# Kernel tuning notes

Measured on AMD Instinct MI355X. Metric: run time of the kernel, lower is better.

The kernel has to match this reference:

```python
import jax, jax.numpy as jnp
import numpy as np
from jax import lax

B, CIN, H, W = 8, 64, 128, 128
COUT, K = 128, 3
PAD, STRIDE, DIL = 1, 1, 1
KK = K * K


def setup_inputs() -> dict:
    ks = jax.random.split(jax.random.key(0), 6)
    x = jax.random.normal(ks[0], (B, CIN, H, W), jnp.float32)
    pre_w = jax.random.normal(ks[1], (CIN, CIN, 1, 1), jnp.float32) * (1.0 / float(np.sqrt(CIN)))
    pre_b = jnp.zeros((CIN,), jnp.float32)
    off_w = jax.random.normal(ks[2], (2 * KK, CIN, K, K), jnp.float32) * 0.01
    off_b = jnp.zeros((2 * KK,), jnp.float32)
    mod_w = jax.random.normal(ks[3], (KK, CIN, K, K), jnp.float32) * 0.01
    mod_b = jnp.zeros((KK,), jnp.float32)
    reg_w = jax.random.normal(ks[4], (COUT, CIN, K, K), jnp.float32) * (1.0 / float(np.sqrt(CIN * KK)))
    return dict(x=x, pre_w=pre_w, pre_b=pre_b, off_w=off_w, off_b=off_b,
                mod_w=mod_w, mod_b=mod_b, reg_w=reg_w)


def _conv3x3(x, w, b):
    y = lax.conv_general_dilated(x, w, (STRIDE, STRIDE), [(PAD, PAD), (PAD, PAD)],
                                 rhs_dilation=(DIL, DIL),
                                 dimension_numbers=('NCHW', 'OIHW', 'NCHW'))
    return y + b[None, :, None, None]


def _bilinear(img, py, px):
    # img: [C,H,W]; py,px: [KK,Ho,Wo] float coords; zero padding outside image
    Hh, Ww = img.shape[1], img.shape[2]
    y0f = jnp.floor(py)
    x0f = jnp.floor(px)
    wy = py - y0f
    wx = px - x0f
    y0 = y0f.astype(jnp.int32)
    x0 = x0f.astype(jnp.int32)

    def gather(yi, xi):
        valid = (yi >= 0) & (yi < Hh) & (xi >= 0) & (xi < Ww)
        yc = jnp.clip(yi, 0, Hh - 1)
        xc = jnp.clip(xi, 0, Ww - 1)
        return img[:, yc, xc] * valid[None].astype(img.dtype)  # [C,KK,Ho,Wo]

    return (gather(y0, x0) * ((1 - wy) * (1 - wx))[None]
            + gather(y0, x0 + 1) * ((1 - wy) * wx)[None]
            + gather(y0 + 1, x0) * (wy * (1 - wx))[None]
            + gather(y0 + 1, x0 + 1) * (wy * wx)[None])


def _dcn_forward(x, pre_w, pre_b, off_w, off_b, mod_w, mod_b, reg_w):
    # 1x1 channel-mapping conv created in the original forward
    x = lax.conv_general_dilated(x, pre_w, (1, 1), 'VALID',
                                 dimension_numbers=('NCHW', 'OIHW', 'NCHW'))
    x = x + pre_b[None, :, None, None]

    offset = _conv3x3(x, off_w, off_b)                    # [B,2*KK,Ho,Wo]
    mask = 2.0 * jax.nn.sigmoid(_conv3x3(x, mod_w, mod_b))  # [B,KK,Ho,Wo]

    Ho, Wo = offset.shape[2], offset.shape[3]
    off = offset.reshape(B, KK, 2, Ho, Wo)  # torchvision layout: per kernel pos (dy,dx)

    ky, kx = jnp.meshgrid(jnp.arange(K), jnp.arange(K), indexing='ij')
    base_y = (jnp.arange(Ho) * STRIDE - PAD)[None, :, None] + (ky.reshape(KK) * DIL)[:, None, None]  # [KK,Ho,1]
    base_x = (jnp.arange(Wo) * STRIDE - PAD)[None, None, :] + (kx.reshape(KK) * DIL)[:, None, None]  # [KK,1,Wo]

    py = base_y[None].astype(x.dtype) + off[:, :, 0]  # [B,KK,Ho,Wo]
    px = base_x[None].astype(x.dtype) + off[:, :, 1]

    sampled = jax.vmap(_bilinear)(x, py, px)          # [B,C,KK,Ho,Wo]
    sampled = sampled * mask[:, None]                  # modulation

    wk = reg_w.reshape(COUT, CIN, KK)
    return jnp.einsum('bckhw,ock->bohw', sampled, wk)  # [B,COUT,Ho,Wo]


def reference(x, pre_w, pre_b, off_w, off_b, mod_w, mod_b, reg_w):
    return _dcn_forward(x, pre_w, pre_b, off_w, off_b, mod_w, mod_b, reg_w)
```

## Files before the change

kernel.cpp:

```cpp
#include <hip/hip_runtime.h>
#include <hip/hip_bf16.h>
#include <cstdint>
#include <cstddef>

#define BATCH 8
#define CINC  64
#define HH    128
#define WWW   128
#define COUTC 128
#define KKC   9
#define KDIM  576
#define HWC   (HH*WWW)
#define NPX   (BATCH*HWC)

#define AT_BASE 98304
#define AT_SZ   32768

typedef float f32x4 __attribute__((ext_vector_type(4)));
typedef short bf16x8 __attribute__((ext_vector_type(8)));

static __device__ __forceinline__ unsigned short f2bf(float f){
    unsigned u = __builtin_bit_cast(unsigned, f);
    u += 0x7fffu + ((u >> 16) & 1u);
    return (unsigned short)(u >> 16);
}
static __device__ __forceinline__ float bf_lo(unsigned u){
    return __builtin_bit_cast(float, u << 16);
}
static __device__ __forceinline__ float bf_hi(unsigned u){
    return __builtin_bit_cast(float, u & 0xffff0000u);
}
static __device__ __forceinline__ unsigned cvtpk(float lo, float hi){
    unsigned r;
    asm("v_cvt_pk_bf16_f32 %0, %1, %2" : "=v"(r) : "v"(lo), "v"(hi));
    return r;
}

__global__ __launch_bounds__(256) void prep_weights(
        const float* __restrict__ off_w, const float* __restrict__ mod_w,
        const float* __restrict__ reg_w, const float* __restrict__ pre_w,
        unsigned short* __restrict__ Wb, unsigned short* __restrict__ Wc,
        unsigned short* __restrict__ Wp)
{
    int idx = blockIdx.x * 256 + threadIdx.x;
    if (idx < COUTC * KDIM) {
        int o = idx / KDIM, k = idx % KDIM;
        int kk = k >> 6, c = k & 63;
        Wb[idx] = f2bf(reg_w[(o * CINC + c) * KKC + kk]);
    }
    int idx2 = idx - COUTC * KDIM;
    if (idx2 >= 0 && idx2 < 32 * KDIM) {
        int o = idx2 / KDIM, k = idx2 % KDIM;
        int kk = k >> 6, c = k & 63;
        float v = 0.f;
        if (o < 18)      v = off_w[(o * CINC + c) * KKC + kk];
        else if (o < 27) v = mod_w[((o - 18) * CINC + c) * KKC + kk];
        Wc[idx2] = f2bf(v);
    }
    int idx3 = idx - (COUTC * KDIM + 32 * KDIM);
    if (idx3 >= 0 && idx3 < CINC * CINC)
        Wp[idx3] = f2bf(pre_w[idx3]);
}

__global__ __launch_bounds__(256) void conv1x1(
        const float* __restrict__ x, const unsigned short* __restrict__ Wp,
        const float* __restrict__ pre_b, unsigned short* __restrict__ xp)
{
    __shared__ unsigned short slab[4][64 * 72];

    const int tid = threadIdx.x;
    const int lane = tid & 63;
    const int wv   = tid >> 6;
    const int l15  = lane & 15;
    const int l4   = lane >> 4;

    int bid = (int)blockIdx.x;
    int bswz = (bid & 7) * 64 + (bid >> 3);
    int pxb = bswz * 256 + wv * 64;
    int b = pxb >> 14, hw0 = pxb & 16383;
    const float* xb = x + (size_t)b * CINC * HWC + hw0;

    bf16x8 bw[4][2];
    #pragma unroll
    for (int fn = 0; fn < 4; ++fn)
        #pragma unroll
        for (int s = 0; s < 2; ++s)
            bw[fn][s] = *(const bf16x8*)(Wp + (size_t)(16*fn + l15) * 64 + 32*s + 8*l4);
    float pb[4];
    #pragma unroll
    for (int fn = 0; fn < 4; ++fn) pb[fn] = pre_b[16*fn + l15];

    f32x4 acc[4][4];
    #pragma unroll
    for (int su = 0; su < 4; ++su)
        #pragma unroll
        for (int fn = 0; fn < 4; ++fn) acc[su][fn] = (f32x4){0.f,0.f,0.f,0.f};

    #pragma unroll
    for (int su = 0; su < 4; ++su) {
        #pragma unroll
        for (int s = 0; s < 2; ++s) {
            float f[8];
            #pragma unroll
            for (int j = 0; j < 8; ++j)
                f[j] = xb[(size_t)(s*32 + 8*l4 + j) * HWC + su*16 + l15];
            unsigned pk[4];
            #pragma unroll
            for (int d = 0; d < 4; ++d) pk[d] = cvtpk(f[2*d], f[2*d+1]);
            bf16x8 A = __builtin_bit_cast(bf16x8, make_uint4(pk[0], pk[1], pk[2], pk[3]));
            #pragma unroll
            for (int fn = 0; fn < 4; ++fn)
                acc[su][fn] = __builtin_amdgcn_mfma_f32_16x16x32_bf16(A, bw[fn][s], acc[su][fn], 0,0,0);
        }
    }

    unsigned short* sl = slab[wv];
    #pragma unroll
    for (int su = 0; su < 4; ++su)
        #pragma unroll
        for (int fn = 0; fn < 4; ++fn)
            #pragma unroll
            for (int r = 0; r < 4; ++r)
                sl[(su*16 + 4*l4 + r) * 72 + 16*fn + l15] = f2bf(acc[su][fn][r] + pb[fn]);
    const uint4* srow = (const uint4*)(sl + lane * 72);
    uint4* drow = (uint4*)(xp + (size_t)(pxb + lane) * 64);
    #pragma unroll
    for (int q = 0; q < 8; ++q) drow[q] = srow[q];
}

__global__ __launch_bounds__(512, 2) void gather_einsum(
        const unsigned short* __restrict__ xp,
        const unsigned short* __restrict__ Wb,
        const unsigned short* __restrict__ Wc,
        const float* __restrict__ off_b,
        const float* __restrict__ mod_b,
        float* __restrict__ out)
{
    __shared__ char smem[163840];
    char* winc = smem;
    float* epi = (float*)smem;

    const int tid  = (int)threadIdx.x;
    const int lane = tid & 63;
    const int wv   = tid >> 6;
    const int l15  = lane & 15;
    const int l4   = lane >> 4;

    int bid = (int)blockIdx.x;
    int bswz = (bid & 7) * 64 + (bid >> 3);
    const int b  = bswz >> 6;
    const int h0 = (bswz & 63) * 2;

    const unsigned short* xpb = xp + (size_t)b * HWC * CINC;

    #pragma unroll
    for (int i = 0; i < 12; ++i) {
        int c = i * 512 + tid;
        int r = c >> 10;
        int c10 = c & 1023;
        int xph = c10 >> 3, g = c10 & 7;
        int y = h0 - 2 + r;
        uint4 v = make_uint4(0u,0u,0u,0u);
        if ((unsigned)y < 128u)
            v = *(const uint4*)(xpb + ((size_t)y * 128 + xph) * 64 + g * 8);
        *(uint4*)(winc + (r*128 + xph)*128 + ((g ^ (xph & 7)) << 4)) = v;
    }
    __syncthreads();

    const int hrow = wv >> 2;
    const int x0w  = (wv & 3) * 32;
    {
        f32x4 aco[2][2];
        #pragma unroll
        for (int j = 0; j < 2; ++j)
            #pragma unroll
            for (int fn = 0; fn < 2; ++fn) aco[j][fn] = (f32x4){0.f,0.f,0.f,0.f};

        #pragma unroll
        for (int kk = 0; kk < 9; ++kk) {
            bf16x8 bc0[2], bc1[2];
            #pragma unroll
            for (int fn = 0; fn < 2; ++fn) {
                bc0[fn] = *(const bf16x8*)(Wc + (size_t)(16*fn + l15) * KDIM + kk*64 + 8*l4);
                bc1[fn] = *(const bf16x8*)(Wc + (size_t)(16*fn + l15) * KDIM + kk*64 + 32 + 8*l4);
            }
            int wr_ = hrow + (kk / 3) + 1;
            #pragma unroll
            for (int j = 0; j < 2; ++j) {
                int xx = x0w + j*16 + l15 + (kk % 3) - 1;
                bool xv = (unsigned)xx < 128u;
                int xc = xx < 0 ? 0 : (xx > 127 ? 127 : xx);
                int sx = xc & 7;
                const char* rr = winc + (wr_*128 + xc)*128;
                uint4 a0 = *(const uint4*)(rr + ((l4 ^ sx) << 4));
                uint4 a1 = *(const uint4*)(rr + (((l4+4) ^ sx) << 4));
                if (!xv) { a0 = make_uint4(0,0,0,0); a1 = make_uint4(0,0,0,0); }
                bf16x8 A0 = __builtin_bit_cast(bf16x8, a0);
                bf16x8 A1 = __builtin_bit_cast(bf16x8, a1);
                #pragma unroll
                for (int fn = 0; fn < 2; ++fn) {
                    aco[j][fn] = __builtin_amdgcn_mfma_f32_16x16x32_bf16(A0, bc0[fn], aco[j][fn], 0,0,0);
                    aco[j][fn] = __builtin_amdgcn_mfma_f32_16x16x32_bf16(A1, bc1[fn], aco[j][fn], 0,0,0);
                }
            }
        }
        float* Dt = (float*)(smem + AT_BASE);
        #pragma unroll
        for (int j = 0; j < 2; ++j)
        #pragma unroll
        for (int fn = 0; fn < 2; ++fn) {
            int o = 16*fn + l15;
            #pragma unroll
            for (int r = 0; r < 4; ++r) {
                int pr = 4*l4 + r;
                int px = wv*32 + j*16 + pr;
                float v = aco[j][fn][r];
                if (o < 18) {
                    v += off_b[o];
                    int k = o >> 1;
                    if ((o & 1) == 0) v += (float)(h0 + hrow - 1 + k/3);
                    else              v += (float)(x0w + j*16 + pr - 1 + (k % 3));
                } else if (o < 27) {
                    v = 2.f / (1.f + __expf(-(v + mod_b[o - 18])));
                }
                if (o < 27) Dt[px*29 + o] = v;
            }
        }
    }
    __syncthreads();

    float cy[2][9], cx[2][9], cm[2][9];
    {
        const float* Dt = (const float*)(smem + AT_BASE);
        #pragma unroll
        for (int j = 0; j < 2; ++j) {
            int px = wv*32 + j*16 + l15;
            #pragma unroll
            for (int kk = 0; kk < 9; ++kk) {
                cy[j][kk] = Dt[px*29 + 2*kk];
                cx[j][kk] = Dt[px*29 + 2*kk + 1];
                cm[j][kk] = Dt[px*29 + 18 + kk];
            }
        }
    }
    __syncthreads();

    f32x4 acc[8][2];
    #pragma unroll
    for (int m = 0; m < 8; ++m) { acc[m][0] = (f32x4){0.f,0.f,0.f,0.f};
                                  acc[m][1] = (f32x4){0.f,0.f,0.f,0.f}; }

    const int wr = wv >> 2, wc = wv & 3;
    const unsigned short* wrow = Wb + (size_t)(32*wc + l15) * KDIM + 8*l4;
    const int sw  = l15 & 7;
    const int ao1 = (l4 ^ sw) << 4, ao2 = ((l4 + 4) ^ sw) << 4;

    #define LERP_TILE(kk_)  do {                                              \
        char* Ab = smem + AT_BASE + ((kk_) & 1) * AT_SZ;                      \
        _Pragma("unroll")                                                     \
        for (int j = 0; j < 2; ++j) {                                         \
            float Y = cy[j][kk_], X = cx[j][kk_], M = cm[j][kk_];             \
            float yf = floorf(Y), xf = floorf(X);                             \
            float wy = Y - yf, wx = X - xf;                                   \
            int y0 = (int)yf, x0i = (int)xf;                                  \
            int y1 = y0 + 1, x1 = x0i + 1;                                    \
            bool yv0 = (unsigned)y0 < 128u, yv1 = (unsigned)y1 < 128u;        \
            bool xv0 = (unsigned)x0i < 128u, xv1 = (unsigned)x1 < 128u;       \
            int xc0 = x0i < 0 ? 0 : (x0i > 127 ? 127 : x0i);                  \
            int xc1 = x1  < 0 ? 0 : (x1  > 127 ? 127 : x1);                   \
            int wr0 = y0 - (h0 - 2), wr1 = wr0 + 1;                           \
            int wc0 = wr0 < 0 ? 0 : (wr0 > 5 ? 5 : wr0);                      \
            int wc1 = wr1 < 0 ? 0 : (wr1 > 5 ? 5 : wr1);                      \
            int s0 = xc0 & 7, s1 = xc1 & 7;                                   \
            const char* r00 = winc + (wc0*128 + xc0)*128;                     \
            const char* r01 = winc + (wc0*128 + xc1)*128;                     \
            const char* r10 = winc + (wc1*128 + xc0)*128;                     \
            const char* r11 = winc + (wc1*128 + xc1)*128;                     \
            uint4 cb0 = *(const uint4*)(r00 + ((l4 ^ s0) << 4));              \
            uint4 cb1 = *(const uint4*)(r00 + (((l4+4) ^ s0) << 4));          \
            uint4 cb2 = *(const uint4*)(r01 + ((l4 ^ s1) << 4));              \
            uint4 cb3 = *(const uint4*)(r01 + (((l4+4) ^ s1) << 4));          \
            uint4 cb4 = *(const uint4*)(r10 + ((l4 ^ s0) << 4));              \
            uint4 cb5 = *(const uint4*)(r10 + (((l4+4) ^ s0) << 4));          \
            uint4 cb6 = *(const uint4*)(r11 + ((l4 ^ s1) << 4));              \
            uint4 cb7 = *(const uint4*)(r11 + (((l4+4) ^ s1) << 4));          \
            bool oob = (yv0 && (unsigned)wr0 > 5u) || (yv1 && (unsigned)wr1 > 5u); \
            if (__builtin_expect(oob, 0)) {                                   \
                int yc0 = y0 < 0 ? 0 : (y0 > 127 ? 127 : y0);                 \
                int yc1 = y1 < 0 ? 0 : (y1 > 127 ? 127 : y1);                 \
                const unsigned short* p00 = xpb + (size_t)(yc0*128 + xc0)*64 + 8*l4; \
                const unsigned short* p01 = xpb + (size_t)(yc0*128 + xc1)*64 + 8*l4; \
                const unsigned short* p10 = xpb + (size_t)(yc1*128 + xc0)*64 + 8*l4; \
                const unsigned short* p11 = xpb + (size_t)(yc1*128 + xc1)*64 + 8*l4; \
                cb0 = *(const uint4*)(p00);  cb1 = *(const uint4*)(p00 + 32); \
                cb2 = *(const uint4*)(p01);  cb3 = *(const uint4*)(p01 + 32); \
                cb4 = *(const uint4*)(p10);  cb5 = *(const uint4*)(p10 + 32); \
                cb6 = *(const uint4*)(p11);  cb7 = *(const uint4*)(p11 + 32); \
            }                                                                 \
            float u00 = (1.f - wy) * (1.f - wx) * M * ((yv0 && xv0) ? 1.f : 0.f); \
            float u01 = (1.f - wy) * wx         * M * ((yv0 && xv1) ? 1.f : 0.f); \
            float u10 = wy * (1.f - wx)         * M * ((yv1 && xv0) ? 1.f : 0.f); \
            float u11 = wy * wx                 * M * ((yv1 && xv1) ? 1.f : 0.f); \
            unsigned pk0[4], pk1[4];                                          \
            _Pragma("unroll")                                                 \
            for (int d = 0; d < 4; ++d) {                                     \
                unsigned q00, q01, q10, q11;                                  \
                q00 = cb0[d]; q01 = cb2[d]; q10 = cb4[d]; q11 = cb6[d];       \
                {                                                             \
                    float slo = bf_lo(q00)*u00 + bf_lo(q01)*u01 + bf_lo(q10)*u10 + bf_lo(q11)*u11; \
                    float shi = bf_hi(q00)*u00 + bf_hi(q01)*u01 + bf_hi(q10)*u10 + bf_hi(q11)*u11; \
                    pk0[d] = cvtpk(slo, shi);                                 \
                }                                                             \
                q00 = cb1[d]; q01 = cb3[d]; q10 = cb5[d]; q11 = cb7[d];       \
                {                                                             \
                    float slo = bf_lo(q00)*u00 + bf_lo(q01)*u01 + bf_lo(q10)*u10 + bf_lo(q11)*u11; \
                    float shi = bf_hi(q00)*u00 + bf_hi(q01)*u01 + bf_hi(q10)*u10 + bf_hi(q11)*u11; \
                    pk1[d] = cvtpk(slo, shi);                                 \
                }                                                             \
            }                                                                 \
            int pxl = wv*32 + j*16 + l15;                                     \
            char* ab = Ab + pxl*128;                                          \
            *(uint4*)(ab + ao1) = make_uint4(pk0[0], pk0[1], pk0[2], pk0[3]); \
            *(uint4*)(ab + ao2) = make_uint4(pk1[0], pk1[1], pk1[2], pk1[3]); \
        }                                                                     \
    } while (0)

    #define GEMM_STEP(g_)  do {                                               \
        const char* Ab = smem + AT_BASE + ((g_) & 1) * AT_SZ;                 \
        bf16x8 Bf00 = *(const bf16x8*)(wrow + (g_)*64);                       \
        bf16x8 Bf01 = *(const bf16x8*)(wrow + (g_)*64 + 32);                  \
        bf16x8 Bf10 = *(const bf16x8*)(wrow + (size_t)16*KDIM + (g_)*64);     \
        bf16x8 Bf11 = *(const bf16x8*)(wrow + (size_t)16*KDIM + (g_)*64 + 32);\
        _Pragma("unroll")                                                     \
        for (int m = 0; m < 8; ++m) {                                         \
            const char* ar = Ab + (128*wr + 16*m + l15)*128;                  \
            bf16x8 A0 = *(const bf16x8*)(ar + ao1);                           \
            bf16x8 A1 = *(const bf16x8*)(ar + ao2);                           \
            acc[m][0] = __builtin_amdgcn_mfma_f32_16x16x32_bf16(A0, Bf00, acc[m][0], 0,0,0); \
            acc[m][0] = __builtin_amdgcn_mfma_f32_16x16x32_bf16(A1, Bf01, acc[m][0], 0,0,0); \
            acc[m][1] = __builtin_amdgcn_mfma_f32_16x16x32_bf16(A0, Bf10, acc[m][1], 0,0,0); \
            acc[m][1] = __builtin_amdgcn_mfma_f32_16x16x32_bf16(A1, Bf11, acc[m][1], 0,0,0); \
        }                                                                     \
    } while (0)

    LERP_TILE(0);
    __syncthreads();
    #pragma unroll 1
    for (int kk = 1; kk < 9; ++kk) {
        LERP_TILE(kk);
        GEMM_STEP(kk - 1);
        __syncthreads();
    }
    GEMM_STEP(8);
    __syncthreads();

    #undef LERP_TILE
    #undef GEMM_STEP

    #pragma unroll
    for (int m = 0; m < 8; ++m)
        #pragma unroll
        for (int f = 0; f < 2; ++f)
            *(f32x4*)(epi + (size_t)(32*wc + 16*f + l15) * 260 + 128*wr + 16*m + 4*l4) = acc[m][f];
    __syncthreads();

    float* ob = out + (size_t)b * COUTC * HWC + h0 * 128;
    #pragma unroll
    for (int it = 0; it < 16; ++it) {
        int idx = it * 512 + tid;
        int o = idx >> 6, c = idx & 63;
        f32x4 v = *(const f32x4*)(epi + (size_t)o * 260 + 4*c);
        *(f32x4*)(ob + (size_t)o * HWC + 4*c) = v;
    }
}

extern "C" void kernel_launch(void* const* d_in, const int* in_sizes, int n_in,
                              void* d_out, int out_size, void* d_ws, size_t ws_size,
                              hipStream_t stream)
{
    const float* x     = (const float*)d_in[0];
    const float* pre_w = (const float*)d_in[1];
    const float* pre_b = (const float*)d_in[2];
    const float* off_w = (const float*)d_in[3];
    const float* off_b = (const float*)d_in[4];
    const float* mod_w = (const float*)d_in[5];
    const float* mod_b = (const float*)d_in[6];
    const float* reg_w = (const float*)d_in[7];
    float* out = (float*)d_out;

    unsigned short* xp = (unsigned short*)d_ws;
    unsigned short* Wb = (unsigned short*)((char*)d_ws + 16777216);
    unsigned short* Wc = (unsigned short*)((char*)d_ws + 16924672);
    unsigned short* Wp = (unsigned short*)((char*)d_ws + 16961536);

    prep_weights<<<dim3(376), dim3(256), 0, stream>>>(off_w, mod_w, reg_w, pre_w, Wb, Wc, Wp);
    conv1x1     <<<dim3(512), dim3(256), 0, stream>>>(x, Wp, pre_b, xp);
    gather_einsum<<<dim3(512), dim3(512), 0, stream>>>(xp, Wb, Wc, off_b, mod_b, out);
}
```

Measured before the change: 103.9 us.

## Halve gather_einsum tile width to fit two blocks per CU

The fused deformable-conv kernel now tiles 2 rows x 64 columns per block with 256 threads and 1024 blocks, instead of 2 rows x 128 columns with 512 threads. The LDS input window and the epilogue buffer shrink so that two independent blocks can share a CU, letting one block's barriers and sampling overlap with another's MFMA work. The offset/mask 3x3 conv now reads its inputs straight from global memory rather than the LDS window. In exchange, the 64-wide window has no horizontal halo, so samples at tile column edges fall into the slower global-memory gather path, and the offset-conv loads lose LDS reuse.

```diff
diff --git a/kernel.cpp b/kernel.cpp
--- a/kernel.cpp
+++ b/kernel.cpp
@@ -13,8 +13,11 @@
 #define HWC   (HH*WWW)
 #define NPX   (BATCH*HWC)
 
-#define AT_BASE 98304
-#define AT_SZ   32768
+#define WIN_W   64
+#define WIN_SZ  (6*WIN_W*128)
+#define AT_BASE WIN_SZ
+#define AT_SZ   (128*128)
+#define LDS_SZ  (WIN_SZ + 2*AT_SZ)
 
 typedef float f32x4 __attribute__((ext_vector_type(4)));
 typedef short bf16x8 __attribute__((ext_vector_type(8)));
@@ -128,7 +131,7 @@
     for (int q = 0; q < 8; ++q) drow[q] = srow[q];
 }
 
-__global__ __launch_bounds__(512, 2) void gather_einsum(
+__global__ __launch_bounds__(256, 2) void gather_einsum(
         const unsigned short* __restrict__ xp,
         const unsigned short* __restrict__ Wb,
         const unsigned short* __restrict__ Wc,
@@ -136,7 +139,7 @@
         const float* __restrict__ mod_b,
         float* __restrict__ out)
 {
-    __shared__ char smem[163840];
+    __shared__ char smem[LDS_SZ];
     char* winc = smem;
     float* epi = (float*)smem;
 
@@ -147,28 +150,29 @@
     const int l4   = lane >> 4;
 
     int bid = (int)blockIdx.x;
-    int bswz = (bid & 7) * 64 + (bid >> 3);
-    const int b  = bswz >> 6;
-    const int h0 = (bswz & 63) * 2;
+    int bswz = (bid & 7) * 128 + (bid >> 3);
+    const int b   = bswz >> 7;
+    const int rem = bswz & 127;
+    const int h0  = (rem >> 1) << 1;
+    const int x0w = (rem & 1) << 6;
 
     const unsigned short* xpb = xp + (size_t)b * HWC * CINC;
 
     #pragma unroll
     for (int i = 0; i < 12; ++i) {
-        int c = i * 512 + tid;
-        int r = c >> 10;
-        int c10 = c & 1023;
-        int xph = c10 >> 3, g = c10 & 7;
+        int c = i * 256 + tid;
+        int r = c >> 9;
+        int cr = c & 511;
+        int wx = cr >> 3, g = cr & 7;
         int y = h0 - 2 + r;
         uint4 v = make_uint4(0u,0u,0u,0u);
         if ((unsigned)y < 128u)
-            v = *(const uint4*)(xpb + ((size_t)y * 128 + xph) * 64 + g * 8);
-        *(uint4*)(winc + (r*128 + xph)*128 + ((g ^ (xph & 7)) << 4)) = v;
-    }
-    __syncthreads();
-
-    const int hrow = wv >> 2;
-    const int x0w  = (wv & 3) * 32;
+            v = *(const uint4*)(xpb + ((size_t)y * 128 + x0w + wx) * 64 + g * 8);
+        *(uint4*)(winc + (r*WIN_W + wx)*128 + ((g ^ (wx & 7)) << 4)) = v;
+    }
+
+    const int hrow = wv >> 1;
+    const int xsl  = (wv & 1) * 32;
     {
         f32x4 aco[2][2];
         #pragma unroll
@@ -184,17 +188,17 @@
                 bc0[fn] = *(const bf16x8*)(Wc + (size_t)(16*fn + l15) * KDIM + kk*64 + 8*l4);
                 bc1[fn] = *(const bf16x8*)(Wc + (size_t)(16*fn + l15) * KDIM + kk*64 + 32 + 8*l4);
             }
-            int wr_ = hrow + (kk / 3) + 1;
+            int y = h0 + hrow + kk/3 - 1;
+            bool yv = (unsigned)y < 128u;
             #pragma unroll
             for (int j = 0; j < 2; ++j) {
-                int xx = x0w + j*16 + l15 + (kk % 3) - 1;
-                bool xv = (unsigned)xx < 128u;
-                int xc = xx < 0 ? 0 : (xx > 127 ? 127 : xx);
-                int sx = xc & 7;
-                const char* rr = winc + (wr_*128 + xc)*128;
-                uint4 a0 = *(const uint4*)(rr + ((l4 ^ sx) << 4));
-                uint4 a1 = *(const uint4*)(rr + (((l4+4) ^ sx) << 4));
-                if (!xv) { a0 = make_uint4(0,0,0,0); a1 = make_uint4(0,0,0,0); }
+                int gx = x0w + xsl + j*16 + l15 + kk%3 - 1;
+                bool val = yv && ((unsigned)gx < 128u);
+                const uint4* src = (const uint4*)(xpb
+                    + ((size_t)((y & 127) * 128 + (gx & 127))) * 64 + 8 * l4);
+                uint4 z = make_uint4(0u,0u,0u,0u);
+                uint4 a0 = val ? src[0] : z;
+                uint4 a1 = val ? src[4] : z;
                 bf16x8 A0 = __builtin_bit_cast(bf16x8, a0);
                 bf16x8 A1 = __builtin_bit_cast(bf16x8, a1);
                 #pragma unroll
@@ -213,17 +217,17 @@
             #pragma unroll
             for (int r = 0; r < 4; ++r) {
                 int pr = 4*l4 + r;
-                int px = wv*32 + j*16 + pr;
+                int p  = hrow*64 + xsl + j*16 + pr;
                 float v = aco[j][fn][r];
                 if (o < 18) {
                     v += off_b[o];
                     int k = o >> 1;
                     if ((o & 1) == 0) v += (float)(h0 + hrow - 1 + k/3);
-                    else              v += (float)(x0w + j*16 + pr - 1 + (k % 3));
+                    else              v += (float)(x0w + xsl + j*16 + pr - 1 + (k % 3));
                 } else if (o < 27) {
                     v = 2.f / (1.f + __expf(-(v + mod_b[o - 18])));
                 }
-                if (o < 27) Dt[px*29 + o] = v;
+                if (o < 27) Dt[p*29 + o] = v;
             }
         }
     }
@@ -234,12 +238,12 @@
         const float* Dt = (const float*)(smem + AT_BASE);
         #pragma unroll
         for (int j = 0; j < 2; ++j) {
-            int px = wv*32 + j*16 + l15;
+            int p = wv*32 + j*16 + l15;
             #pragma unroll
             for (int kk = 0; kk < 9; ++kk) {
-                cy[j][kk] = Dt[px*29 + 2*kk];
-                cx[j][kk] = Dt[px*29 + 2*kk + 1];
-                cm[j][kk] = Dt[px*29 + 18 + kk];
+                cy[j][kk] = Dt[p*29 + 2*kk];
+                cx[j][kk] = Dt[p*29 + 2*kk + 1];
+                cm[j][kk] = Dt[p*29 + 18 + kk];
             }
         }
     }
@@ -250,8 +254,7 @@
     for (int m = 0; m < 8; ++m) { acc[m][0] = (f32x4){0.f,0.f,0.f,0.f};
                                   acc[m][1] = (f32x4){0.f,0.f,0.f,0.f}; }
 
-    const int wr = wv >> 2, wc = wv & 3;
-    const unsigned short* wrow = Wb + (size_t)(32*wc + l15) * KDIM + 8*l4;
+    const unsigned short* wrow = Wb + (size_t)(32*wv + l15) * KDIM + 8*l4;
     const int sw  = l15 & 7;
     const int ao1 = (l4 ^ sw) << 4, ao2 = ((l4 + 4) ^ sw) << 4;
 
@@ -266,16 +269,19 @@
             int y1 = y0 + 1, x1 = x0i + 1;                                    \
             bool yv0 = (unsigned)y0 < 128u, yv1 = (unsigned)y1 < 128u;        \
             bool xv0 = (unsigned)x0i < 128u, xv1 = (unsigned)x1 < 128u;       \
-            int xc0 = x0i < 0 ? 0 : (x0i > 127 ? 127 : x0i);                  \
-            int xc1 = x1  < 0 ? 0 : (x1  > 127 ? 127 : x1);                   \
             int wr0 = y0 - (h0 - 2), wr1 = wr0 + 1;                           \
+            int wxi = x0i - x0w;                                              \
+            bool inW0 = (unsigned)wxi < (unsigned)WIN_W;                      \
+            bool inW1 = (unsigned)(wxi + 1) < (unsigned)WIN_W;                \
             int wc0 = wr0 < 0 ? 0 : (wr0 > 5 ? 5 : wr0);                      \
             int wc1 = wr1 < 0 ? 0 : (wr1 > 5 ? 5 : wr1);                      \
-            int s0 = xc0 & 7, s1 = xc1 & 7;                                   \
-            const char* r00 = winc + (wc0*128 + xc0)*128;                     \
-            const char* r01 = winc + (wc0*128 + xc1)*128;                     \
-            const char* r10 = winc + (wc1*128 + xc0)*128;                     \
-            const char* r11 = winc + (wc1*128 + xc1)*128;                     \
+            int wx0 = wxi < 0 ? 0 : (wxi > WIN_W-1 ? WIN_W-1 : wxi);          \
+            int wx1 = wxi+1 < 0 ? 0 : (wxi+1 > WIN_W-1 ? WIN_W-1 : wxi+1);    \
+            int s0 = wx0 & 7, s1 = wx1 & 7;                                   \
+            const char* r00 = winc + (wc0*WIN_W + wx0)*128;                   \
+            const char* r01 = winc + (wc0*WIN_W + wx1)*128;                   \
+            const char* r10 = winc + (wc1*WIN_W + wx0)*128;                   \
+            const char* r11 = winc + (wc1*WIN_W + wx1)*128;                   \
             uint4 cb0 = *(const uint4*)(r00 + ((l4 ^ s0) << 4));              \
             uint4 cb1 = *(const uint4*)(r00 + (((l4+4) ^ s0) << 4));          \
             uint4 cb2 = *(const uint4*)(r01 + ((l4 ^ s1) << 4));              \
@@ -284,10 +290,13 @@
             uint4 cb5 = *(const uint4*)(r10 + (((l4+4) ^ s0) << 4));          \
             uint4 cb6 = *(const uint4*)(r11 + ((l4 ^ s1) << 4));              \
             uint4 cb7 = *(const uint4*)(r11 + (((l4+4) ^ s1) << 4));          \
-            bool oob = (yv0 && (unsigned)wr0 > 5u) || (yv1 && (unsigned)wr1 > 5u); \
+            bool oob = (yv0 && (unsigned)wr0 > 5u) || (yv1 && (unsigned)wr1 > 5u) \
+                    || (xv0 && !inW0) || (xv1 && !inW1);                      \
             if (__builtin_expect(oob, 0)) {                                   \
                 int yc0 = y0 < 0 ? 0 : (y0 > 127 ? 127 : y0);                 \
                 int yc1 = y1 < 0 ? 0 : (y1 > 127 ? 127 : y1);                 \
+                int xc0 = x0i < 0 ? 0 : (x0i > 127 ? 127 : x0i);              \
+                int xc1 = x1  < 0 ? 0 : (x1  > 127 ? 127 : x1);               \
                 const unsigned short* p00 = xpb + (size_t)(yc0*128 + xc0)*64 + 8*l4; \
                 const unsigned short* p01 = xpb + (size_t)(yc0*128 + xc1)*64 + 8*l4; \
                 const unsigned short* p10 = xpb + (size_t)(yc1*128 + xc0)*64 + 8*l4; \
@@ -318,8 +327,8 @@
                     pk1[d] = cvtpk(slo, shi);                                 \
                 }                                                             \
             }                                                                 \
-            int pxl = wv*32 + j*16 + l15;                                     \
-            char* ab = Ab + pxl*128;                                          \
+            int p = wv*32 + j*16 + l15;                                       \
+            char* ab = Ab + p*128;                                            \
             *(uint4*)(ab + ao1) = make_uint4(pk0[0], pk0[1], pk0[2], pk0[3]); \
             *(uint4*)(ab + ao2) = make_uint4(pk1[0], pk1[1], pk1[2], pk1[3]); \
         }                                                                     \
@@ -333,7 +342,7 @@
         bf16x8 Bf11 = *(const bf16x8*)(wrow + (size_t)16*KDIM + (g_)*64 + 32);\
         _Pragma("unroll")                                                     \
         for (int m = 0; m < 8; ++m) {                                         \
-            const char* ar = Ab + (128*wr + 16*m + l15)*128;                  \
+            const char* ar = Ab + (16*m + l15)*128;                           \
             bf16x8 A0 = *(const bf16x8*)(ar + ao1);                           \
             bf16x8 A1 = *(const bf16x8*)(ar + ao2);                           \
             acc[m][0] = __builtin_amdgcn_mfma_f32_16x16x32_bf16(A0, Bf00, acc[m][0], 0,0,0); \
@@ -361,16 +370,17 @@
     for (int m = 0; m < 8; ++m)
         #pragma unroll
         for (int f = 0; f < 2; ++f)
-            *(f32x4*)(epi + (size_t)(32*wc + 16*f + l15) * 260 + 128*wr + 16*m + 4*l4) = acc[m][f];
+            *(f32x4*)(epi + (size_t)(32*wv + 16*f + l15) * 130 + 16*m + 4*l4) = acc[m][f];
     __syncthreads();
 
-    float* ob = out + (size_t)b * COUTC * HWC + h0 * 128;
+    float* ob = out + (size_t)b * COUTC * HWC + h0 * 128 + x0w;
     #pragma unroll
     for (int it = 0; it < 16; ++it) {
-        int idx = it * 512 + tid;
-        int o = idx >> 6, c = idx & 63;
-        f32x4 v = *(const f32x4*)(epi + (size_t)o * 260 + 4*c);
-        *(f32x4*)(ob + (size_t)o * HWC + 4*c) = v;
+        int idx = it * 256 + tid;
+        int o = idx >> 5, q = idx & 31;
+        int p = 4 * q;
+        f32x4 v = *(const f32x4*)(epi + (size_t)o * 130 + p);
+        *(f32x4*)(ob + (size_t)o * HWC + (p >> 6) * 128 + (p & 63)) = v;
     }
 }
 
@@ -395,5 +405,5 @@
 
     prep_weights<<<dim3(376), dim3(256), 0, stream>>>(off_w, mod_w, reg_w, pre_w, Wb, Wc, Wp);
     conv1x1     <<<dim3(512), dim3(256), 0, stream>>>(x, Wp, pre_b, xp);
-    gather_einsum<<<dim3(512), dim3(512), 0, stream>>>(xp, Wb, Wc, off_b, mod_b, out);
-}
+    gather_einsum<<<dim3(1024), dim3(256), 0, stream>>>(xp, Wb, Wc, off_b, mod_b, out);
+}
```

Result: slower. 121.4 us (+16.8%).
